# Performance work log

Hardware: AMD Instinct MI355X
Metric: run time of the kernel (lower is better)

Reference implementation:

```python
import jax, jax.numpy as jnp
import numpy as np

KS = 3          # kernel_size
NUM_FA = 16     # number of functional atoms per pixel
TOTAL_BASES = 6 # num_bases * (ks // 2)
BN_EPS = 1e-5


def _conv3x3(x, w, b):
    # NCHW conv, padding=1, stride=1
    y = jax.lax.conv_general_dilated(
        x, w, window_strides=(1, 1), padding=[(1, 1), (1, 1)],
        dimension_numbers=("NCHW", "OIHW", "NCHW"))
    return y + b[None, :, None, None]


def _bn(x, gamma, beta, mean, var):
    scale = gamma / jnp.sqrt(var + BN_EPS)
    return (x - mean[None, :, None, None]) * scale[None, :, None, None] + beta[None, :, None, None]


def setup_inputs() -> dict:
    key = jax.random.key(0)
    ks = jax.random.split(key, 16)
    N, C, H, W = 16, 64, 64, 64
    INTER, BC_DIM, O = 64, TOTAL_BASES * NUM_FA, 128
    f32 = jnp.float32
    return {
        "x": jax.random.normal(ks[0], (N, C, H, W), f32),
        "conv1_w": jax.random.normal(ks[1], (INTER, C, 3, 3), f32) * 0.05,
        "conv1_b": jax.random.normal(ks[2], (INTER,), f32) * 0.05,
        "bn1_gamma": jax.random.uniform(ks[3], (INTER,), f32, 0.5, 1.5),
        "bn1_beta": jax.random.normal(ks[4], (INTER,), f32) * 0.05,
        "bn1_mean": jax.random.normal(ks[5], (INTER,), f32) * 0.05,
        "bn1_var": jax.random.uniform(ks[6], (INTER,), f32, 0.5, 1.5),
        "conv2_w": jax.random.normal(ks[7], (BC_DIM, INTER, 3, 3), f32) * 0.05,
        "conv2_b": jax.random.normal(ks[8], (BC_DIM,), f32) * 0.05,
        "bn2_gamma": jax.random.uniform(ks[9], (BC_DIM,), f32, 0.5, 1.5),
        "bn2_beta": jax.random.normal(ks[10], (BC_DIM,), f32) * 0.05,
        "bn2_mean": jax.random.normal(ks[11], (BC_DIM,), f32) * 0.05,
        "bn2_var": jax.random.uniform(ks[12], (BC_DIM,), f32, 0.5, 1.5),
        "bases": jax.random.normal(ks[13], (TOTAL_BASES, KS * KS), f32),
        "coef": jax.random.normal(ks[14], (O, C * NUM_FA), f32) * 0.02,
    }


def reference(x, conv1_w, conv1_b, bn1_gamma, bn1_beta, bn1_mean, bn1_var,
              conv2_w, conv2_b, bn2_gamma, bn2_beta, bn2_mean, bn2_var,
              bases, coef):
    N, C, H, W = x.shape
    # bases_net: conv3x3 -> BN -> tanh -> conv3x3 -> BN -> tanh
    h = jnp.tanh(_bn(_conv3x3(x, conv1_w, conv1_b), bn1_gamma, bn1_beta, bn1_mean, bn1_var))
    bc = jnp.tanh(_bn(_conv3x3(h, conv2_w, conv2_b), bn2_gamma, bn2_beta, bn2_mean, bn2_var))
    # torch: .transpose(1,-1).view(N,H,W,num_fa,total_bases)  (swaps H/W; H==W)
    bases_coef = jnp.transpose(bc, (0, 3, 2, 1)).reshape(N, H, W, NUM_FA, TOTAL_BASES)
    # atoms: (bases_coef[...,None] * bases).sum(-2).transpose(-1,-2) -> (N,H,W,ks2,num_fa)
    atoms = jnp.einsum("nhwft,tk->nhwkf", bases_coef, bases)
    # unfold(x, ks, padding=1) -> patches (N,H,W,C,ks2), channel-major like torch unfold
    xp = jnp.pad(x, ((0, 0), (0, 0), (1, 1), (1, 1)))
    patches = jnp.stack([xp[:, :, i:i + H, j:j + W] for i in range(KS) for j in range(KS)], axis=2)  # (N,C,9,H,W)
    patches = jnp.transpose(patches, (0, 3, 4, 1, 2))  # (N,H,W,C,9)
    # (x.unsqueeze(-1) * atoms.unsqueeze(-3)).sum(-2) -> (N,H,W,C,num_fa) -> flatten C-major
    bases_out = jnp.einsum("nhwck,nhwkf->nhwcf", patches, atoms).reshape(N, H, W, C * NUM_FA)
    # torch: .transpose(1,-1) -> (N, C*num_fa, W, H), then 1x1 conv with coef
    out = jnp.einsum("nhwd,od->nowh", bases_out, coef)  # (N, O, W, H)
    return out
```

## Files before the change

### kernel.cpp

```cpp
#include <hip/hip_runtime.h>
#include <math.h>
#include <string.h>

#define NBATCH 16

typedef __attribute__((ext_vector_type(8))) short short8;
typedef __attribute__((ext_vector_type(4))) float floatx4;
#define MFMA16(a, b, c) __builtin_amdgcn_mfma_f32_16x16x32_bf16(a, b, c, 0, 0, 0)

#define GLOAD(dst, ptr, offlit)                                   \
  asm volatile("global_load_dwordx4 %0, %1, off offset:" offlit   \
               : "=&v"(dst)                                       \
               : "v"(ptr)                                         \
               : "memory")

__device__ __forceinline__ unsigned int cvtpk(float a, float b) {
  unsigned int r;
  asm("v_cvt_pk_bf16_f32 %0, %1, %2" : "=v"(r) : "v"(a), "v"(b));
  return r;
}
__device__ __forceinline__ unsigned short f2bf(float f) {
  return (unsigned short)(cvtpk(f, 0.f) & 0xffffu);
}
__device__ __forceinline__ unsigned int packbf2(float a, float b) {
  return cvtpk(a, b);
}
__device__ __forceinline__ float bflo(unsigned int u) {
  return __uint_as_float(u << 16);
}
__device__ __forceinline__ float bfhi(unsigned int u) {
  return __uint_as_float(u & 0xffff0000u);
}
__device__ __forceinline__ float fast_tanh(float x) {
  float e = __expf(2.f * x);
  return 1.f - 2.f / (e + 1.f);
}

__global__ __launch_bounds__(256) void prep_all(
    const float* __restrict__ x, unsigned short* __restrict__ xb,
    const float* __restrict__ w1, const float* __restrict__ w2,
    const float* __restrict__ coef, unsigned short* __restrict__ w1swz,
    unsigned short* __restrict__ w2swz, unsigned short* __restrict__ coefswz) {
  __shared__ float tile[64][65];
  const int t = threadIdx.x;
  if (blockIdx.x < 64) {
    const int y = blockIdx.x, n = blockIdx.y;
    const float* xn = x + (size_t)n * 64 * 4096 + y * 64;
#pragma unroll
    for (int it = 0; it < 16; ++it) {
      int idx = it * 256 + t;
      int c = idx >> 6, xx = idx & 63;
      tile[c][xx] = xn[c * 4096 + xx];
    }
    __syncthreads();
    const int xx = t >> 2, cq = t & 3;
    unsigned short* dst = xb + ((size_t)n * 4096 + y * 64 + xx) * 64;
#pragma unroll
    for (int jj = 0; jj < 2; ++jj) {
      int ch0 = cq * 16 + jj * 8;
      unsigned int p[4];
#pragma unroll
      for (int e = 0; e < 4; ++e)
        p[e] = packbf2(tile[ch0 + e * 2][xx], tile[ch0 + e * 2 + 1][xx]);
      *(uint4*)&dst[ch0] = make_uint4(p[0], p[1], p[2], p[3]);
    }
    return;
  }
  int i = ((blockIdx.x - 64) * NBATCH + blockIdx.y) * 256 + t;
  if (i < 131072) {
    int j = i & 7, f = i >> 3;
    int lane = f & 63;
    int u = (f >> 6) & 3;
    int wj = (f >> 8) & 1;
    int kc = (f >> 9) & 1;
    int rd = f >> 10;
    int lm = lane & 15, lq = lane >> 4;
    int oc = wj * 64 + u * 16 + lm;
    int k = rd * 64 + kc * 32 + lq * 8 + j;
    coefswz[i] = f2bf(coef[oc * 1024 + k]);
  }
  if (i < 36864) {
    int j = i & 7, f = i >> 3;
    int lane = f & 63;
    int u = (f >> 6) & 1;
    int wn = (f >> 7) & 1;
    int kc = (f >> 8) & 1;
    int off = f >> 9;
    int lm = lane & 15, lq = lane >> 4;
    int oc = wn * 32 + u * 16 + lm;
    int ic = kc * 32 + lq * 8 + j;
    w1swz[i] = f2bf(w1[(oc * 64 + ic) * 9 + off]);
  }
  if (i < 55296) {
    int j = i & 7, f = i >> 3;
    int lane = f & 63;
    int rem = f >> 6;
    int u = rem % 3;
    int rem2 = rem / 3;
    int wn = rem2 & 1;
    int kc = (rem2 >> 1) & 1;
    int off = rem2 >> 2;
    int lm = lane & 15, lq = lane >> 4;
    int oc = wn * 48 + u * 16 + lm;
    int ic = kc * 32 + lq * 8 + j;
    w2swz[i] = f2bf(w2[(oc * 64 + ic) * 9 + off]);
  }
}

__global__ __launch_bounds__(256, 2) void mega(
    const unsigned short* __restrict__ xb, const unsigned short* __restrict__ w1swz,
    const unsigned short* __restrict__ w2swz, const float* __restrict__ b1,
    const float* __restrict__ g1, const float* __restrict__ be1,
    const float* __restrict__ m1, const float* __restrict__ v1,
    const float* __restrict__ b2, const float* __restrict__ g2,
    const float* __restrict__ be2, const float* __restrict__ m2,
    const float* __restrict__ v2, const float* __restrict__ bases,
    const unsigned short* __restrict__ coefswz, float* __restrict__ out) {
  __shared__ unsigned short xls[144 * 72];
  __shared__ unsigned short hls[100 * 72];
  __shared__ unsigned short lbc[64 * 96];
  __shared__ unsigned short As[4 * 1024];
  __shared__ unsigned short xs[100 * 72];

  const int t = threadIdx.x;
  const int tile = blockIdx.x, n = blockIdx.y;
  const int x0 = (tile & 7) * 8, y0 = (tile >> 3) * 8;
  const int q0 = y0, p0 = x0;

  const unsigned short* xbn = xb + (size_t)n * 4096 * 64;

#pragma unroll
  for (int it = 0; it < 5; ++it) {
    int idx = it * 256 + t;
    if (idx < 1152) {
      int pos = idx >> 3, u4 = idx & 7;
      int xr = pos / 12, xc = pos - xr * 12;
      int gy = y0 - 2 + xr, gx = x0 - 2 + xc;
      uint4 v = {0u, 0u, 0u, 0u};
      if ((unsigned)gy < 64u && (unsigned)gx < 64u)
        v = *(const uint4*)&xbn[((size_t)gy * 64 + gx) * 64 + u4 * 8];
      *(uint4*)&xls[pos * 72 + u4 * 8] = v;
    }
  }
#pragma unroll
  for (int it = 0; it < 4; ++it) {
    int idx = it * 256 + t;
    if (idx < 800) {
      int pos = idx >> 3, u4 = idx & 7;
      int row = pos / 10, col = pos - row * 10;
      int gp = p0 - 1 + row, gq = q0 - 1 + col;
      uint4 v = {0u, 0u, 0u, 0u};
      if ((unsigned)gp < 64u && (unsigned)gq < 64u)
        v = *(const uint4*)&xbn[((size_t)gp * 64 + gq) * 64 + u4 * 8];
      *(uint4*)&xs[pos * 72 + u4 * 8] = v;
    }
  }
  __syncthreads();

  const int lane = t & 63, w = t >> 6;
  const int wm = w & 1, wn = w >> 1;
  const int lm = lane & 15, lq = lane >> 4;

  {
    int abase[4];
#pragma unroll
    for (int i = 0; i < 4; ++i) {
      int px = (wm + 2 * i) * 16 + lm;
      if (px > 99) px = 99;
      int hr = px / 10, hc = px - hr * 10;
      abase[i] = (hr * 12 + hc) * 72 + lq * 8;
    }
    floatx4 acc[4][2];
#pragma unroll
    for (int i = 0; i < 4; ++i)
#pragma unroll
      for (int u = 0; u < 2; ++u) acc[i][u] = floatx4{0.f, 0.f, 0.f, 0.f};

#pragma unroll
    for (int step = 0; step < 18; ++step) {
      const int off = step >> 1, kc = step & 1;
      const int di = off / 3, dj = off % 3;
      short8 b[2];
#pragma unroll
      for (int u = 0; u < 2; ++u)
        b[u] = *(const short8*)&w1swz[(off * 512 + kc * 256 + wn * 128 +
                                       u * 64 + lane) * 8];
#pragma unroll
      for (int i = 0; i < 4; ++i) {
        short8 a =
            *(const short8*)&xls[abase[i] + (di * 12 + dj) * 72 + kc * 32];
        acc[i][0] = MFMA16(a, b[0], acc[i][0]);
        acc[i][1] = MFMA16(a, b[1], acc[i][1]);
      }
    }
    float sc[2], sh[2];
#pragma unroll
    for (int u = 0; u < 2; ++u) {
      int oc = wn * 32 + u * 16 + lm;
      sc[u] = g1[oc] * rsqrtf(v1[oc] + 1e-5f);
      sh[u] = (b1[oc] - m1[oc]) * sc[u] + be1[oc];
    }
#pragma unroll
    for (int i = 0; i < 4; ++i) {
      int px0 = (wm + 2 * i) * 16 + lq * 4;
#pragma unroll
      for (int u = 0; u < 2; ++u) {
        int oc = wn * 32 + u * 16 + lm;
#pragma unroll
        for (int r = 0; r < 4; ++r) {
          int px = px0 + r;
          if (px < 100) {
            int hr = px / 10, hc = px - hr * 10;
            int gy = y0 - 1 + hr, gx = x0 - 1 + hc;
            bool valid = ((unsigned)gy < 64u) && ((unsigned)gx < 64u);
            float val = valid ? fast_tanh(acc[i][u][r] * sc[u] + sh[u]) : 0.f;
            hls[px * 72 + oc] = f2bf(val);
          }
        }
      }
    }
  }
  __syncthreads();

  {
    int hbase[2];
#pragma unroll
    for (int s = 0; s < 2; ++s) {
      int opx = (wm + 2 * s) * 16 + lm;
      int yl = opx >> 3, xl = opx & 7;
      hbase[s] = (yl * 10 + xl) * 72 + lq * 8;
    }
    floatx4 acc2[2][3];
#pragma unroll
    for (int s = 0; s < 2; ++s)
#pragma unroll
      for (int u = 0; u < 3; ++u) acc2[s][u] = floatx4{0.f, 0.f, 0.f, 0.f};

#pragma unroll
    for (int step = 0; step < 18; ++step) {
      const int off = step >> 1, kc = step & 1;
      const int di = off / 3, dj = off % 3;
      short8 b[3];
#pragma unroll
      for (int u = 0; u < 3; ++u)
        b[u] = *(const short8*)&w2swz[(off * 768 + kc * 384 + wn * 192 +
                                       u * 64 + lane) * 8];
#pragma unroll
      for (int s = 0; s < 2; ++s) {
        short8 a =
            *(const short8*)&hls[hbase[s] + (di * 10 + dj) * 72 + kc * 32];
        acc2[s][0] = MFMA16(a, b[0], acc2[s][0]);
        acc2[s][1] = MFMA16(a, b[1], acc2[s][1]);
        acc2[s][2] = MFMA16(a, b[2], acc2[s][2]);
      }
    }
    float sc[3], sh[3];
#pragma unroll
    for (int u = 0; u < 3; ++u) {
      int oc = wn * 48 + u * 16 + lm;
      sc[u] = g2[oc] * rsqrtf(v2[oc] + 1e-5f);
      sh[u] = (b2[oc] - m2[oc]) * sc[u] + be2[oc];
    }
#pragma unroll
    for (int s = 0; s < 2; ++s) {
      int opx0 = (wm + 2 * s) * 16 + lq * 4;
#pragma unroll
      for (int u = 0; u < 3; ++u) {
        int oc = wn * 48 + u * 16 + lm;
#pragma unroll
        for (int r = 0; r < 4; ++r) {
          int opx = opx0 + r;
          lbc[opx * 96 + oc] = f2bf(fast_tanh(acc2[s][u][r] * sc[u] + sh[u]));
        }
      }
    }
  }
  __syncthreads();

  float bs[54];
#pragma unroll
  for (int i = 0; i < 54; ++i) bs[i] = bases[i];

  const int pxl_b = lane >> 2, fh4 = lane & 3;
  const int px_b = w * 16 + pxl_b;
  const int qx_b = px_b >> 3, py_b = px_b & 7;

  float atf[9][4];
  {
    const unsigned short* bp = &lbc[px_b * 96 + fh4 * 24];
    float bcv[24];
#pragma unroll
    for (int m = 0; m < 3; ++m) {
      uint4 v = *(const uint4*)(bp + m * 8);
      unsigned int uu[4] = {v.x, v.y, v.z, v.w};
#pragma unroll
      for (int e = 0; e < 4; ++e) {
        bcv[m * 8 + e * 2] = bflo(uu[e]);
        bcv[m * 8 + e * 2 + 1] = bfhi(uu[e]);
      }
    }
#pragma unroll
    for (int j = 0; j < 4; ++j)
#pragma unroll
      for (int k = 0; k < 9; ++k) {
        float s0 = 0.f;
#pragma unroll
        for (int tt = 0; tt < 6; ++tt)
          s0 = fmaf(bcv[j * 6 + tt], bs[tt * 9 + k], s0);
        atf[k][j] = s0;
      }
  }

  int pa[9];
#pragma unroll
  for (int i = 0; i < 3; ++i)
#pragma unroll
    for (int j = 0; j < 3; ++j)
      pa[i * 3 + j] = ((py_b + i) * 10 + qx_b + j) * 72;

  floatx4 acc[2][4];
#pragma unroll
  for (int wj = 0; wj < 2; ++wj)
#pragma unroll
    for (int u = 0; u < 4; ++u) acc[wj][u] = floatx4{0.f, 0.f, 0.f, 0.f};

  unsigned short* Asw = &As[w * 1024];

  uint2 qv[9];
  auto qload = [&](int rd) {
    const int coff = rd * 4;
#pragma unroll
    for (int p = 0; p < 9; ++p) qv[p] = *(const uint2*)&xs[pa[p] + coff];
  };
  auto build = [&]() {
    float a[4][4];
    {
      float c0 = bflo(qv[0].x), c1 = bfhi(qv[0].x);
      float c2 = bflo(qv[0].y), c3 = bfhi(qv[0].y);
#pragma unroll
      for (int j = 0; j < 4; ++j) {
        float av = atf[0][j];
        a[0][j] = c0 * av;
        a[1][j] = c1 * av;
        a[2][j] = c2 * av;
        a[3][j] = c3 * av;
      }
    }
#pragma unroll
    for (int p = 1; p < 9; ++p) {
      float c0 = bflo(qv[p].x), c1 = bfhi(qv[p].x);
      float c2 = bflo(qv[p].y), c3 = bfhi(qv[p].y);
#pragma unroll
      for (int j = 0; j < 4; ++j) {
        float av = atf[p][j];
        a[0][j] = fmaf(c0, av, a[0][j]);
        a[1][j] = fmaf(c1, av, a[1][j]);
        a[2][j] = fmaf(c2, av, a[2][j]);
        a[3][j] = fmaf(c3, av, a[3][j]);
      }
    }
#pragma unroll
    for (int cc = 0; cc < 4; ++cc) {
      int g = (cc * 4 + fh4) ^ ((pxl_b & 7) << 1);
      uint2 val;
      val.x = cvtpk(a[cc][0], a[cc][1]);
      val.y = cvtpk(a[cc][2], a[cc][3]);
      *(uint2*)&Asw[pxl_b * 64 + g * 4] = val;
    }
  };

  qload(0);
  build();

  for (int rd = 0; rd < 16; ++rd) {
    short8 Bf[2][2][4];
    {
      const unsigned short* b0 = coefswz + (size_t)rd * 8192 + lane * 8;
      const unsigned short* b1 = b0 + 2048;
      const unsigned short* b2 = b0 + 4096;
      const unsigned short* b3 = b0 + 6144;
      GLOAD(Bf[0][0][0], b0, "0");
      GLOAD(Bf[0][0][1], b0, "1024");
      GLOAD(Bf[0][0][2], b0, "2048");
      GLOAD(Bf[0][0][3], b0, "3072");
      GLOAD(Bf[0][1][0], b1, "0");
      GLOAD(Bf[0][1][1], b1, "1024");
      GLOAD(Bf[0][1][2], b1, "2048");
      GLOAD(Bf[0][1][3], b1, "3072");
      GLOAD(Bf[1][0][0], b2, "0");
      GLOAD(Bf[1][0][1], b2, "1024");
      GLOAD(Bf[1][0][2], b2, "2048");
      GLOAD(Bf[1][0][3], b2, "3072");
      GLOAD(Bf[1][1][0], b3, "0");
      GLOAD(Bf[1][1][1], b3, "1024");
      GLOAD(Bf[1][1][2], b3, "2048");
      GLOAD(Bf[1][1][3], b3, "3072");
    }
    short8 Af[2];
#pragma unroll
    for (int kc = 0; kc < 2; ++kc) {
      int u16 = (kc * 4 + lq) ^ (lm & 7);
      Af[kc] = *(const short8*)&Asw[lm * 64 + u16 * 8];
    }
    __builtin_amdgcn_sched_barrier(0);
    if (rd < 15) {
      qload(rd + 1);
      build();
    }
    asm volatile("s_waitcnt vmcnt(0)" ::: "memory");
    __builtin_amdgcn_sched_barrier(0);
    __builtin_amdgcn_s_setprio(1);
#pragma unroll
    for (int kc = 0; kc < 2; ++kc)
#pragma unroll
      for (int wj = 0; wj < 2; ++wj)
#pragma unroll
        for (int u = 0; u < 4; ++u)
          acc[wj][u] = MFMA16(Af[kc], Bf[kc][wj][u], acc[wj][u]);
    __builtin_amdgcn_s_setprio(0);
  }

  float* outn = out + (size_t)n * 128 * 4096;
#pragma unroll
  for (int wj = 0; wj < 2; ++wj)
#pragma unroll
    for (int u = 0; u < 4; ++u) {
      int oc = wj * 64 + u * 16 + lm;
      int gpx = w * 16 + lq * 4;
      int qx = gpx >> 3, py0 = gpx & 7;
      *(float4*)&outn[((size_t)oc * 64 + q0 + qx) * 64 + p0 + py0] =
          make_float4(acc[wj][u][0], acc[wj][u][1], acc[wj][u][2],
                      acc[wj][u][3]);
    }
}

extern "C" void kernel_launch(void* const* d_in, const int* in_sizes, int n_in,
                              void* d_out, int out_size, void* d_ws,
                              size_t ws_size, hipStream_t stream) {
  const float* x = (const float*)d_in[0];
  const float* conv1_w = (const float*)d_in[1];
  const float* conv1_b = (const float*)d_in[2];
  const float* bn1_g = (const float*)d_in[3];
  const float* bn1_b = (const float*)d_in[4];
  const float* bn1_m = (const float*)d_in[5];
  const float* bn1_v = (const float*)d_in[6];
  const float* conv2_w = (const float*)d_in[7];
  const float* conv2_b = (const float*)d_in[8];
  const float* bn2_g = (const float*)d_in[9];
  const float* bn2_b = (const float*)d_in[10];
  const float* bn2_m = (const float*)d_in[11];
  const float* bn2_v = (const float*)d_in[12];
  const float* bases = (const float*)d_in[13];
  const float* coef = (const float*)d_in[14];
  float* out = (float*)d_out;

  char* ws = (char*)d_ws;
  unsigned short* xbuf = (unsigned short*)(ws);
  unsigned short* w1swz = (unsigned short*)(ws + 20971520);
  unsigned short* w2swz = (unsigned short*)(ws + 21045248);
  unsigned short* coefswz = (unsigned short*)(ws + 21155840);

  prep_all<<<dim3(96, NBATCH), 256, 0, stream>>>(x, xbuf, conv1_w, conv2_w,
                                                 coef, w1swz, w2swz, coefswz);
  mega<<<dim3(64, NBATCH), 256, 0, stream>>>(
      xbuf, w1swz, w2swz, conv1_b, bn1_g, bn1_b, bn1_m, bn1_v, conv2_b, bn2_g,
      bn2_b, bn2_m, bn2_v, bases, coefswz, out);
}
```

Before: 169.1 us.

## Split final GEMM across waves by output channel with shared double-buffered A tile

The final 1x1-conv GEMM previously had each wave own 16 pixels and load the full 128-channel coefficient slice per round. Now each wave owns 32 output channels across all 64 pixels of the block. The A tile (atoms times patches) is built cooperatively into a double-buffered shared buffer, with a block barrier each round. This cuts per-wave global coefficient loads fourfold, at the cost of more LDS reads per wave and a __syncthreads in every iteration.

```diff
diff --git a/kernel.cpp b/kernel.cpp
--- a/kernel.cpp
+++ b/kernel.cpp
@@ -119,7 +119,7 @@
   __shared__ unsigned short xls[144 * 72];
   __shared__ unsigned short hls[100 * 72];
   __shared__ unsigned short lbc[64 * 96];
-  __shared__ unsigned short As[4 * 1024];
+  __shared__ unsigned short As[2 * 4096];
   __shared__ unsigned short xs[100 * 72];
 
   const int t = threadIdx.x;
@@ -281,8 +281,7 @@
 #pragma unroll
   for (int i = 0; i < 54; ++i) bs[i] = bases[i];
 
-  const int pxl_b = lane >> 2, fh4 = lane & 3;
-  const int px_b = w * 16 + pxl_b;
+  const int px_b = t >> 2, fh4 = t & 3;
   const int qx_b = px_b >> 3, py_b = px_b & 7;
 
   float atf[9][4];
@@ -318,13 +317,11 @@
     for (int j = 0; j < 3; ++j)
       pa[i * 3 + j] = ((py_b + i) * 10 + qx_b + j) * 72;
 
-  floatx4 acc[2][4];
-#pragma unroll
-  for (int wj = 0; wj < 2; ++wj)
-#pragma unroll
-    for (int u = 0; u < 4; ++u) acc[wj][u] = floatx4{0.f, 0.f, 0.f, 0.f};
-
-  unsigned short* Asw = &As[w * 1024];
+  floatx4 acc[4][2];
+#pragma unroll
+  for (int s = 0; s < 4; ++s)
+#pragma unroll
+    for (int u = 0; u < 2; ++u) acc[s][u] = floatx4{0.f, 0.f, 0.f, 0.f};
 
   uint2 qv[9];
   auto qload = [&](int rd) {
@@ -332,7 +329,7 @@
 #pragma unroll
     for (int p = 0; p < 9; ++p) qv[p] = *(const uint2*)&xs[pa[p] + coff];
   };
-  auto build = [&]() {
+  auto build = [&](int buf) {
     float a[4][4];
     {
       float c0 = bflo(qv[0].x), c1 = bfhi(qv[0].x);
@@ -361,77 +358,73 @@
     }
 #pragma unroll
     for (int cc = 0; cc < 4; ++cc) {
-      int g = (cc * 4 + fh4) ^ ((pxl_b & 7) << 1);
+      int g = (cc * 4 + fh4) ^ ((px_b & 7) << 1);
       uint2 val;
       val.x = cvtpk(a[cc][0], a[cc][1]);
       val.y = cvtpk(a[cc][2], a[cc][3]);
-      *(uint2*)&Asw[pxl_b * 64 + g * 4] = val;
+      *(uint2*)&As[buf * 4096 + px_b * 64 + g * 4] = val;
     }
   };
 
   qload(0);
-  build();
+  build(0);
+  __syncthreads();
 
   for (int rd = 0; rd < 16; ++rd) {
-    short8 Bf[2][2][4];
+    const int buf = rd & 1;
+    short8 Bf[2][2];
     {
-      const unsigned short* b0 = coefswz + (size_t)rd * 8192 + lane * 8;
-      const unsigned short* b1 = b0 + 2048;
-      const unsigned short* b2 = b0 + 4096;
-      const unsigned short* b3 = b0 + 6144;
-      GLOAD(Bf[0][0][0], b0, "0");
-      GLOAD(Bf[0][0][1], b0, "1024");
-      GLOAD(Bf[0][0][2], b0, "2048");
-      GLOAD(Bf[0][0][3], b0, "3072");
-      GLOAD(Bf[0][1][0], b1, "0");
-      GLOAD(Bf[0][1][1], b1, "1024");
-      GLOAD(Bf[0][1][2], b1, "2048");
-      GLOAD(Bf[0][1][3], b1, "3072");
-      GLOAD(Bf[1][0][0], b2, "0");
-      GLOAD(Bf[1][0][1], b2, "1024");
-      GLOAD(Bf[1][0][2], b2, "2048");
-      GLOAD(Bf[1][0][3], b2, "3072");
-      GLOAD(Bf[1][1][0], b3, "0");
-      GLOAD(Bf[1][1][1], b3, "1024");
-      GLOAD(Bf[1][1][2], b3, "2048");
-      GLOAD(Bf[1][1][3], b3, "3072");
-    }
-    short8 Af[2];
-#pragma unroll
-    for (int kc = 0; kc < 2; ++kc) {
-      int u16 = (kc * 4 + lq) ^ (lm & 7);
-      Af[kc] = *(const short8*)&Asw[lm * 64 + u16 * 8];
+      const unsigned short* b0 =
+          coefswz + ((size_t)(rd * 16 + (w >> 1) * 4 + (w & 1) * 2)) * 512 +
+          lane * 8;
+      const unsigned short* b1 = b0 + 4096;
+      GLOAD(Bf[0][0], b0, "0");
+      GLOAD(Bf[0][1], b0, "1024");
+      GLOAD(Bf[1][0], b1, "0");
+      GLOAD(Bf[1][1], b1, "1024");
+    }
+    short8 Af[4][2];
+#pragma unroll
+    for (int s = 0; s < 4; ++s) {
+      int px = s * 16 + lm;
+#pragma unroll
+      for (int kc = 0; kc < 2; ++kc) {
+        int u16 = (kc * 4 + lq) ^ (lm & 7);
+        Af[s][kc] = *(const short8*)&As[buf * 4096 + px * 64 + u16 * 8];
+      }
     }
     __builtin_amdgcn_sched_barrier(0);
     if (rd < 15) {
       qload(rd + 1);
-      build();
-    }
+      build(buf ^ 1);
+    }
+    __builtin_amdgcn_sched_barrier(0);
     asm volatile("s_waitcnt vmcnt(0)" ::: "memory");
+    __syncthreads();
     __builtin_amdgcn_sched_barrier(0);
     __builtin_amdgcn_s_setprio(1);
 #pragma unroll
     for (int kc = 0; kc < 2; ++kc)
 #pragma unroll
-      for (int wj = 0; wj < 2; ++wj)
-#pragma unroll
-        for (int u = 0; u < 4; ++u)
-          acc[wj][u] = MFMA16(Af[kc], Bf[kc][wj][u], acc[wj][u]);
+      for (int u = 0; u < 2; ++u)
+#pragma unroll
+        for (int s = 0; s < 4; ++s)
+          acc[s][u] = MFMA16(Af[s][kc], Bf[kc][u], acc[s][u]);
     __builtin_amdgcn_s_setprio(0);
   }
 
   float* outn = out + (size_t)n * 128 * 4096;
 #pragma unroll
-  for (int wj = 0; wj < 2; ++wj)
-#pragma unroll
-    for (int u = 0; u < 4; ++u) {
-      int oc = wj * 64 + u * 16 + lm;
-      int gpx = w * 16 + lq * 4;
-      int qx = gpx >> 3, py0 = gpx & 7;
+  for (int u = 0; u < 2; ++u) {
+    int oc = w * 32 + u * 16 + lm;
+#pragma unroll
+    for (int s = 0; s < 4; ++s) {
+      int px0 = s * 16 + lq * 4;
+      int qx = px0 >> 3, py0 = px0 & 7;
       *(float4*)&outn[((size_t)oc * 64 + q0 + qx) * 64 + p0 + py0] =
-          make_float4(acc[wj][u][0], acc[wj][u][1], acc[wj][u][2],
-                      acc[wj][u][3]);
-    }
+          make_float4(acc[s][u][0], acc[s][u][1], acc[s][u][2], acc[s][u][3]);
+    }
+  }
 }
 
 extern "C" void kernel_launch(void* const* d_in, const int* in_sizes, int n_in,
```

Result: no change. 171.9 us (+1.7%).
